# Optimization experiments

Hardware: AMD Instinct MI355X
Metric: run time of the kernel (lower is better)

The kernel has to match this reference:

```python
import jax, jax.numpy as jnp
import numpy as np

HEADS = 4
DIM_HEAD = 32
DIM = 128
EPS = 1e-12  # F.normalize eps


def _rmsnorm(t, g):
    # F.normalize over channel dim (dim=1), then * g * sqrt(dim)
    n = jnp.sqrt(jnp.sum(t * t, axis=1, keepdims=True))
    return t / jnp.maximum(n, EPS) * g * (DIM ** 0.5)


def setup_inputs() -> dict:
    key = jax.random.key(0)
    ks = jax.random.split(key, 5)
    b, H, W = 16, 96, 96
    x = jax.random.normal(ks[0], (b, DIM, H, W), dtype=jnp.float32)
    norm_g = jnp.ones((1, DIM, 1, 1), dtype=jnp.float32)
    qkv_w = jax.random.normal(ks[1], (3 * HEADS * DIM_HEAD, DIM), dtype=jnp.float32) * 0.05
    mem_kv = jax.random.normal(ks[2], (2, HEADS, DIM_HEAD, 4), dtype=jnp.float32)
    out_w = jax.random.normal(ks[3], (DIM, HEADS * DIM_HEAD), dtype=jnp.float32) * 0.05
    out_b = jnp.zeros((DIM,), dtype=jnp.float32)
    out_norm_g = jnp.ones((1, DIM, 1, 1), dtype=jnp.float32)
    return {"x": x, "norm_g": norm_g, "qkv_w": qkv_w, "mem_kv": mem_kv,
            "out_w": out_w, "out_b": out_b, "out_norm_g": out_norm_g}


def reference(x, norm_g, qkv_w, mem_kv, out_w, out_b, out_norm_g):
    b, c, H, W = x.shape
    n = H * W
    scale = DIM_HEAD ** (-0.5)

    xn = _rmsnorm(x, norm_g)
    # 1x1 conv (no bias) == channel GEMM
    qkv = jnp.einsum('oc,bchw->bohw', qkv_w, xn)  # [b, 3*h*d, H, W]
    q, k, v = jnp.split(qkv, 3, axis=1)

    def to_heads(t):
        return t.reshape(b, HEADS, DIM_HEAD, n)  # b h d n

    q, k, v = to_heads(q), to_heads(k), to_heads(v)

    mk = jnp.broadcast_to(mem_kv[0], (b, HEADS, DIM_HEAD, mem_kv.shape[-1]))
    mv = jnp.broadcast_to(mem_kv[1], (b, HEADS, DIM_HEAD, mem_kv.shape[-1]))
    k = jnp.concatenate([mk, k], axis=-1)
    v = jnp.concatenate([mv, v], axis=-1)

    q = jax.nn.softmax(q, axis=-2) * scale  # softmax over d
    k = jax.nn.softmax(k, axis=-1)          # softmax over n

    context = jnp.einsum('bhdn,bhen->bhde', k, v)  # [b,h,d,d]
    out = jnp.einsum('bhde,bhdn->bhen', context, q)  # [b,h,d,n]
    out = out.reshape(b, HEADS * DIM_HEAD, H, W)

    out = jnp.einsum('oc,bchw->bohw', out_w, out) + out_b[None, :, None, None]
    return _rmsnorm(out, out_norm_g)
```

## Files before the change

kernel.cpp:

```cpp
#include <hip/hip_runtime.h>
#include <math.h>

#define NPIX 9216
#define NBLK 72
#define TPB 4
#define SCALE 0.17677669529663687f
#define SQRT128 11.313708498984761f

typedef __attribute__((ext_vector_type(8))) short short8;
typedef __attribute__((ext_vector_type(4))) float f32x4;

static __device__ __forceinline__ unsigned short f2bf(float f) {
  union { float f; unsigned u; } v; v.f = f;
  return (unsigned short)((v.u + 0x7fffu + ((v.u >> 16) & 1u)) >> 16);
}
static __device__ __forceinline__ float bf2f(unsigned short h) {
  union { unsigned u; float f; } v; v.u = ((unsigned)h) << 16;
  return v.f;
}


__global__ __launch_bounds__(256) void k_prep2(
    const float* __restrict__ qkv_w, const float* __restrict__ norm_g,
    const float* __restrict__ out_w,
    unsigned short* __restrict__ wbf2, unsigned short* __restrict__ owb2) {
  const int i = blockIdx.x * 256 + threadIdx.x;
  if (i < 6144) {
    const int g = i >> 6, lane = i & 63;
    const int wv = g / 24, rem = g % 24;
    const int mt = rem >> 2, ks = rem & 3;
    const int row = 96 * wv + mt * 16 + (lane & 15);
    const int col = ks * 32 + (lane >> 4) * 8;
    const float* src = qkv_w + row * 128 + col;
    const float* gg = norm_g + col;
    uint4 o;
    o.x = (unsigned)f2bf(src[0] * gg[0]) | ((unsigned)f2bf(src[1] * gg[1]) << 16);
    o.y = (unsigned)f2bf(src[2] * gg[2]) | ((unsigned)f2bf(src[3] * gg[3]) << 16);
    o.z = (unsigned)f2bf(src[4] * gg[4]) | ((unsigned)f2bf(src[5] * gg[5]) << 16);
    o.w = (unsigned)f2bf(src[6] * gg[6]) | ((unsigned)f2bf(src[7] * gg[7]) << 16);
    *(uint4*)(wbf2 + (size_t)i * 8) = o;
  } else if (i < 8192) {
    const int i2 = i - 6144;
    const int g = i2 >> 6, lane = i2 & 63;
    const int wv = g >> 3, rem = g & 7;
    const int mt = rem >> 2, ks = rem & 3;
    const int row = 32 * wv + mt * 16 + (lane & 15);
    const int col = ks * 32 + (lane >> 4) * 8;
    const float* src = out_w + row * 128 + col;
    uint4 o;
    o.x = (unsigned)f2bf(src[0]) | ((unsigned)f2bf(src[1]) << 16);
    o.y = (unsigned)f2bf(src[2]) | ((unsigned)f2bf(src[3]) << 16);
    o.z = (unsigned)f2bf(src[4]) | ((unsigned)f2bf(src[5]) << 16);
    o.w = (unsigned)f2bf(src[6]) | ((unsigned)f2bf(src[7]) << 16);
    *(uint4*)(owb2 + (size_t)i2 * 8) = o;
  }
}

__global__ __launch_bounds__(256) void k_init(const float* __restrict__ mem_kv,
                                              float* __restrict__ ctxG,
                                              float* __restrict__ sumexpG) {
  const int bh = blockIdx.x;
  const int h = bh & 3;
  const float* mk = mem_kv + h * 128;
  const float* mv = mem_kv + 512 + h * 128;
  const int t = threadIdx.x;
  const int d = t >> 3, e0 = (t & 7) * 4;
  float ek[4], se = 0.f;
#pragma unroll
  for (int j = 0; j < 4; ++j) { ek[j] = __expf(mk[d * 4 + j]); se += ek[j]; }
#pragma unroll
  for (int ei = 0; ei < 4; ++ei) {
    const int e = e0 + ei;
    float s = 0.f;
#pragma unroll
    for (int j = 0; j < 4; ++j) s += ek[j] * mv[e * 4 + j];
    ctxG[(bh * 32 + d) * 32 + e] = s;
  }
  if ((t & 7) == 0) sumexpG[bh * 32 + d] = se;
}

template <bool WSQ>
__global__ __launch_bounds__(256, 2) void k1(
    const float* __restrict__ x, const unsigned short* __restrict__ wbf2,
    unsigned short* __restrict__ qb16, float* __restrict__ qf32,
    float* __restrict__ ctx_dst, float* __restrict__ se_dst) {
  __shared__ __align__(16) unsigned char smem[30720 + 4096 + 128];
  unsigned short* qkv = (unsigned short*)smem;
  unsigned short* xnT = (unsigned short*)smem;
  float* redu = (float*)(smem + 30720);
  float* inv = (float*)(smem + 30720 + 4096);

  const int t = threadIdx.x;
  const int b = blockIdx.y;
  const int blk = blockIdx.x;
  const int wv = t >> 6;
  const int lane = t & 63;
  const int lr = lane & 15;
  const int lg = lane >> 4;
  const int r = t >> 3, c4 = (t & 7) * 4;
  const float* xb = x + ((size_t)b * 128) * NPIX + blk * TPB * 32;

  f32x4 acc[6][2];
  f32x4 ctx[2][2];
#pragma unroll
  for (int i = 0; i < 6; ++i)
#pragma unroll
    for (int j = 0; j < 2; ++j)
#pragma unroll
      for (int q = 0; q < 4; ++q) acc[i][j][q] = 0.f;
#pragma unroll
  for (int i = 0; i < 2; ++i)
#pragma unroll
    for (int j = 0; j < 2; ++j)
#pragma unroll
      for (int q = 0; q < 4; ++q) ctx[i][j][q] = 0.f;
  float se_row[2] = {0.f, 0.f};

  float4 pf[4];
#pragma unroll
  for (int pass = 0; pass < 4; ++pass)
    pf[pass] = *(const float4*)(xb + (size_t)(pass * 32 + r) * NPIX + c4);

  for (int it = 0; it < TPB; ++it) {
    const int p0 = (blk * TPB + it) * 32;

    __syncthreads();
    {
      float ss0 = 0.f, ss1 = 0.f, ss2 = 0.f, ss3 = 0.f;
#pragma unroll
      for (int pass = 0; pass < 4; ++pass) {
        const int row = pass * 32 + r;
        const float4 v = pf[pass];
        xnT[(c4 + 0) * 136 + row] = f2bf(v.x);
        xnT[(c4 + 1) * 136 + row] = f2bf(v.y);
        xnT[(c4 + 2) * 136 + row] = f2bf(v.z);
        xnT[(c4 + 3) * 136 + row] = f2bf(v.w);
        ss0 = fmaf(v.x, v.x, ss0); ss1 = fmaf(v.y, v.y, ss1);
        ss2 = fmaf(v.z, v.z, ss2); ss3 = fmaf(v.w, v.w, ss3);
      }
      *(float4*)&redu[r * 32 + c4] = make_float4(ss0, ss1, ss2, ss3);
    }
    __syncthreads();
    {
      short8 bfr[4][2];
#pragma unroll
      for (int ks = 0; ks < 4; ++ks)
#pragma unroll
        for (int nt = 0; nt < 2; ++nt)
          bfr[ks][nt] = *(const short8*)&xnT[(nt * 16 + lr) * 136 + ks * 32 + lg * 8];
      if (it + 1 < TPB) {
        const float* xb2 = xb + (it + 1) * 32;
#pragma unroll
        for (int pass = 0; pass < 4; ++pass)
          pf[pass] = *(const float4*)(xb2 + (size_t)(pass * 32 + r) * NPIX + c4);
      }
      if (t < 32) {
        float s = 0.f;
#pragma unroll
        for (int g = 0; g < 32; ++g) s += redu[g * 32 + t];
        inv[t] = SQRT128 / fmaxf(sqrtf(s), 1e-12f);
      }
      const unsigned short* wbase = wbf2 + (size_t)(wv * 24) * 512 + lane * 8;
#pragma unroll
      for (int mt = 0; mt < 6; ++mt) {
#pragma unroll
        for (int ks = 0; ks < 4; ++ks) {
          const short8 af = *(const short8*)(wbase + (size_t)(mt * 4 + ks) * 512);
          acc[mt][0] = __builtin_amdgcn_mfma_f32_16x16x32_bf16(af, bfr[ks][0], acc[mt][0], 0, 0, 0);
          acc[mt][1] = __builtin_amdgcn_mfma_f32_16x16x32_bf16(af, bfr[ks][1], acc[mt][1], 0, 0, 0);
        }
      }
    }
    __syncthreads();
    {
      const float iv0 = inv[lr], iv1 = inv[16 + lr];
#pragma unroll
      for (int mt = 0; mt < 6; ++mt)
#pragma unroll
        for (int nt = 0; nt < 2; ++nt) {
          const float iv = nt ? iv1 : iv0;
#pragma unroll
          for (int q = 0; q < 4; ++q) {
            const int row = 96 * wv + mt * 16 + lg * 4 + q;
            qkv[row * 40 + nt * 16 + lr] = f2bf(acc[mt][nt][q] * iv);
            acc[mt][nt][q] = 0.f;
          }
        }
    }
    __syncthreads();
    {
      const int c0 = wv * 32 + lg * 8;
#pragma unroll
      for (int px = 0; px < 2; ++px) {
        const int p = px * 16 + lr;
        float qv[8];
#pragma unroll
        for (int j = 0; j < 8; ++j) qv[j] = bf2f(qkv[(c0 + j) * 40 + p]);
        float m = qv[0];
#pragma unroll
        for (int j = 1; j < 8; ++j) m = fmaxf(m, qv[j]);
        m = fmaxf(m, __shfl_xor(m, 16));
        m = fmaxf(m, __shfl_xor(m, 32));
        float s = 0.f;
#pragma unroll
        for (int j = 0; j < 8; ++j) { qv[j] = __expf(qv[j] - m); s += qv[j]; }
        s += __shfl_xor(s, 16);
        s += __shfl_xor(s, 32);
        const float rs = SCALE / s;
        if (WSQ) {
          uint4 qo;
          qo.x = (unsigned)f2bf(qv[0] * rs) | ((unsigned)f2bf(qv[1] * rs) << 16);
          qo.y = (unsigned)f2bf(qv[2] * rs) | ((unsigned)f2bf(qv[3] * rs) << 16);
          qo.z = (unsigned)f2bf(qv[4] * rs) | ((unsigned)f2bf(qv[5] * rs) << 16);
          qo.w = (unsigned)f2bf(qv[6] * rs) | ((unsigned)f2bf(qv[7] * rs) << 16);
          *(uint4*)(qb16 + ((size_t)b * NPIX + p0 + p) * 128 + c0) = qo;
        } else {
#pragma unroll
          for (int j = 0; j < 8; ++j)
            qf32[((size_t)b * 128 + c0 + j) * NPIX + p0 + p] = qv[j] * rs;
        }
      }
      short8 afk[2];
#pragma unroll
      for (int dt = 0; dt < 2; ++dt) {
        const short8 kraw = *(const short8*)&qkv[(128 + wv * 32 + dt * 16 + lr) * 40 + lg * 8];
        short8 e16;
        float s = 0.f;
#pragma unroll
        for (int j = 0; j < 8; ++j) {
          const float ev = __expf(bf2f((unsigned short)kraw[j]));
          e16[j] = (short)f2bf(ev);
          s += ev;
        }
        afk[dt] = e16;
        s += __shfl_xor(s, 16);
        s += __shfl_xor(s, 32);
        se_row[dt] += s;
      }
#pragma unroll
      for (int dt = 0; dt < 2; ++dt)
#pragma unroll
        for (int et = 0; et < 2; ++et) {
          const short8 bf = *(const short8*)&qkv[(256 + wv * 32 + et * 16 + lr) * 40 + lg * 8];
          ctx[dt][et] = __builtin_amdgcn_mfma_f32_16x16x32_bf16(afk[dt], bf, ctx[dt][et], 0, 0, 0);
        }
    }
  }

  if (WSQ) {
    float* dst = ctx_dst + ((size_t)(b * NBLK + blk)) * 4096 + wv * 1024;
#pragma unroll
    for (int dt = 0; dt < 2; ++dt)
#pragma unroll
      for (int et = 0; et < 2; ++et)
#pragma unroll
        for (int q = 0; q < 4; ++q)
          dst[(dt * 16 + lg * 4 + q) * 32 + et * 16 + lr] = ctx[dt][et][q];
    if (lg == 0) {
#pragma unroll
      for (int dt = 0; dt < 2; ++dt)
        se_dst[(b * NBLK + blk) * 128 + wv * 32 + dt * 16 + lr] = se_row[dt];
    }
  } else {
#pragma unroll
    for (int dt = 0; dt < 2; ++dt)
#pragma unroll
      for (int et = 0; et < 2; ++et)
#pragma unroll
        for (int q = 0; q < 4; ++q)
          atomicAdd(&ctx_dst[((size_t)b * 128 + wv * 32 + dt * 16 + lg * 4 + q) * 32 + et * 16 + lr],
                    ctx[dt][et][q]);
    if (lg == 0) {
#pragma unroll
      for (int dt = 0; dt < 2; ++dt)
        atomicAdd(&se_dst[b * 128 + wv * 32 + dt * 16 + lr], se_row[dt]);
    }
  }
}

__global__ __launch_bounds__(256) void k_reduce(
    const float* __restrict__ part_ctx, const float* __restrict__ part_se,
    const float* __restrict__ mem_kv, unsigned short* __restrict__ ctxnT) {
  const int bid = blockIdx.x;
  const int b = bid >> 4, h = (bid >> 2) & 3, dq = bid & 3;
  const int t = threadIdx.x;
  const int dd = t >> 5;
  const int d = dq * 8 + dd;
  const int e = t & 31;
  __shared__ float sise[8];

  const float* mk = mem_kv + h * 128 + d * 4;
  const float* mv = mem_kv + 512 + h * 128 + e * 4;
  float ek[4];
  float acc = 0.f;
#pragma unroll
  for (int j = 0; j < 4; ++j) ek[j] = __expf(mk[j]);
#pragma unroll
  for (int j = 0; j < 4; ++j) acc += ek[j] * mv[j];
  const float* src = part_ctx + (size_t)b * NBLK * 4096 + h * 1024 + d * 32 + e;
  for (int p = 0; p < NBLK; ++p) acc += src[(size_t)p * 4096];
  if (e == 0) {
    float se = ek[0] + ek[1] + ek[2] + ek[3];
    const float* sp = part_se + (size_t)b * NBLK * 128 + h * 32 + d;
    for (int p = 0; p < NBLK; ++p) se += sp[(size_t)p * 128];
    sise[dd] = 1.f / se;
  }
  __syncthreads();
  ctxnT[(size_t)(b * 4 + h) * 1024 + e * 32 + d] = f2bf(acc * sise[dd]);
}

__global__ __launch_bounds__(256) void k_norm(
    const float* __restrict__ ctxG, const float* __restrict__ seG,
    unsigned short* __restrict__ ctxnT) {
  const int b = blockIdx.x;
  const int t = threadIdx.x;
  const int h = t >> 6, d = (t >> 1) & 31, e0 = (t & 1) * 16;
  const int r = h * 32 + d;
  const float ise = 1.f / seG[b * 128 + r];
  const float* src = ctxG + ((size_t)b * 128 + r) * 32;
  unsigned short* dst = ctxnT + ((size_t)(b * 4 + h) * 32) * 32;
#pragma unroll
  for (int i = 0; i < 16; ++i)
    dst[(e0 + i) * 32 + d] = f2bf(src[e0 + i] * ise);
}

__global__ __launch_bounds__(256) void k3_ws(
    const unsigned short* __restrict__ ctxnT, const unsigned short* __restrict__ owb2,
    const unsigned short* __restrict__ qbf, const float* __restrict__ out_b,
    const float* __restrict__ out_norm_g, float* __restrict__ out) {
  __shared__ __align__(16) unsigned char smem[8704 + 2048 + 128];
  unsigned short* o1T = (unsigned short*)smem;
  float* redu = (float*)(smem + 8704);
  float* inv = (float*)(smem + 8704 + 2048);

  const int t = threadIdx.x;
  const int b = blockIdx.y;
  const int p0 = blockIdx.x * 32;
  const int wv = t >> 6;
  const int lane = t & 63;
  const int lr = lane & 15;
  const int lg = lane >> 4;

  {
    f32x4 o1a[2][2];
#pragma unroll
    for (int i = 0; i < 2; ++i)
#pragma unroll
      for (int j = 0; j < 2; ++j)
#pragma unroll
        for (int q = 0; q < 4; ++q) o1a[i][j][q] = 0.f;
    const unsigned short* cbase = ctxnT + (size_t)(b * 4 + wv) * 1024;
    const unsigned short* qb = qbf + ((size_t)b * NPIX + p0) * 128;
    short8 bq[2];
#pragma unroll
    for (int nt = 0; nt < 2; ++nt)
      bq[nt] = *(const short8*)(qb + (size_t)(nt * 16 + lr) * 128 + wv * 32 + lg * 8);
#pragma unroll
    for (int mt = 0; mt < 2; ++mt) {
      const short8 af = *(const short8*)(cbase + (mt * 16 + lr) * 32 + lg * 8);
#pragma unroll
      for (int nt = 0; nt < 2; ++nt)
        o1a[mt][nt] = __builtin_amdgcn_mfma_f32_16x16x32_bf16(af, bq[nt], o1a[mt][nt], 0, 0, 0);
    }
#pragma unroll
    for (int mt = 0; mt < 2; ++mt)
#pragma unroll
      for (int nt = 0; nt < 2; ++nt)
#pragma unroll
        for (int q = 0; q < 4; ++q) {
          const int e = wv * 32 + mt * 16 + lg * 4 + q;
          o1T[(nt * 16 + lr) * 136 + e] = f2bf(o1a[mt][nt][q]);
        }
  }
  __syncthreads();
  f32x4 y[2][2];
#pragma unroll
  for (int i = 0; i < 2; ++i)
#pragma unroll
    for (int j = 0; j < 2; ++j)
#pragma unroll
      for (int q = 0; q < 4; ++q) y[i][j][q] = 0.f;
  const unsigned short* wbase = owb2 + (size_t)(wv * 8) * 512 + lane * 8;
#pragma unroll
  for (int mt = 0; mt < 2; ++mt) {
#pragma unroll
    for (int ks = 0; ks < 4; ++ks) {
      const short8 af = *(const short8*)(wbase + (size_t)(mt * 4 + ks) * 512);
#pragma unroll
      for (int nt = 0; nt < 2; ++nt) {
        const short8 bf = *(const short8*)&o1T[(nt * 16 + lr) * 136 + ks * 32 + lg * 8];
        y[mt][nt] = __builtin_amdgcn_mfma_f32_16x16x32_bf16(af, bf, y[mt][nt], 0, 0, 0);
      }
    }
  }
  {
    float ss[2] = {0.f, 0.f};
#pragma unroll
    for (int mt = 0; mt < 2; ++mt)
#pragma unroll
      for (int q = 0; q < 4; ++q) {
        const int row = 32 * wv + mt * 16 + lg * 4 + q;
        const float bb = out_b[row];
#pragma unroll
        for (int nt = 0; nt < 2; ++nt) {
          y[mt][nt][q] += bb;
          ss[nt] = fmaf(y[mt][nt][q], y[mt][nt][q], ss[nt]);
        }
      }
#pragma unroll
    for (int nt = 0; nt < 2; ++nt)
      redu[(wv * 4 + lg) * 32 + nt * 16 + lr] = ss[nt];
  }
  __syncthreads();
  if (t < 32) {
    float s = 0.f;
#pragma unroll
    for (int g = 0; g < 16; ++g) s += redu[g * 32 + t];
    inv[t] = SQRT128 / fmaxf(sqrtf(s), 1e-12f);
  }
  __syncthreads();
  {
    float* ob = out + (size_t)b * 128 * NPIX + p0;
#pragma unroll
    for (int mt = 0; mt < 2; ++mt)
#pragma unroll
      for (int q = 0; q < 4; ++q) {
        const int row = 32 * wv + mt * 16 + lg * 4 + q;
        const float g = out_norm_g[row];
#pragma unroll
        for (int nt = 0; nt < 2; ++nt) {
          const int col = nt * 16 + lr;
          ob[(size_t)row * NPIX + col] = y[mt][nt][q] * inv[col] * g;
        }
      }
  }
}

__global__ __launch_bounds__(256) void k3f(
    const unsigned short* __restrict__ ctxnT, const unsigned short* __restrict__ owb2,
    const float* __restrict__ out_b, const float* __restrict__ out_norm_g,
    float* __restrict__ io) {
  __shared__ __align__(16) unsigned char smem[8704 + 8704 + 2048 + 128];
  unsigned short* qT = (unsigned short*)smem;
  unsigned short* o1T = (unsigned short*)(smem + 8704);
  float* redu = (float*)(smem + 8704 + 8704);
  float* inv = (float*)(smem + 8704 + 8704 + 2048);

  const int t = threadIdx.x;
  const int b = blockIdx.y;
  const int p0 = blockIdx.x * 32;
  const int wv = t >> 6;
  const int lane = t & 63;
  const int lr = lane & 15;
  const int lg = lane >> 4;

  {
    const float* qb = io + (size_t)b * 128 * NPIX + p0;
    const int r = t >> 3, c4 = (t & 7) * 4;
#pragma unroll
    for (int pass = 0; pass < 4; ++pass) {
      const int row = pass * 32 + r;
      const float4 v = *(const float4*)(qb + (size_t)row * NPIX + c4);
      qT[(c4 + 0) * 136 + row] = f2bf(v.x);
      qT[(c4 + 1) * 136 + row] = f2bf(v.y);
      qT[(c4 + 2) * 136 + row] = f2bf(v.z);
      qT[(c4 + 3) * 136 + row] = f2bf(v.w);
    }
  }
  __syncthreads();
  {
    f32x4 o1a[2][2];
#pragma unroll
    for (int i = 0; i < 2; ++i)
#pragma unroll
      for (int j = 0; j < 2; ++j)
#pragma unroll
        for (int q = 0; q < 4; ++q) o1a[i][j][q] = 0.f;
    const unsigned short* cbase = ctxnT + (size_t)(b * 4 + wv) * 1024;
#pragma unroll
    for (int mt = 0; mt < 2; ++mt) {
      const short8 af = *(const short8*)(cbase + (mt * 16 + lr) * 32 + lg * 8);
#pragma unroll
      for (int nt = 0; nt < 2; ++nt) {
        const short8 bf = *(const short8*)&qT[(nt * 16 + lr) * 136 + wv * 32 + lg * 8];
        o1a[mt][nt] = __builtin_amdgcn_mfma_f32_16x16x32_bf16(af, bf, o1a[mt][nt], 0, 0, 0);
      }
    }
#pragma unroll
    for (int mt = 0; mt < 2; ++mt)
#pragma unroll
      for (int nt = 0; nt < 2; ++nt)
#pragma unroll
        for (int q = 0; q < 4; ++q) {
          const int e = wv * 32 + mt * 16 + lg * 4 + q;
          o1T[(nt * 16 + lr) * 136 + e] = f2bf(o1a[mt][nt][q]);
        }
  }
  __syncthreads();
  f32x4 y[2][2];
#pragma unroll
  for (int i = 0; i < 2; ++i)
#pragma unroll
    for (int j = 0; j < 2; ++j)
#pragma unroll
      for (int q = 0; q < 4; ++q) y[i][j][q] = 0.f;
  const unsigned short* wbase = owb2 + (size_t)(wv * 8) * 512 + lane * 8;
#pragma unroll
  for (int mt = 0; mt < 2; ++mt) {
#pragma unroll
    for (int ks = 0; ks < 4; ++ks) {
      const short8 af = *(const short8*)(wbase + (size_t)(mt * 4 + ks) * 512);
#pragma unroll
      for (int nt = 0; nt < 2; ++nt) {
        const short8 bf = *(const short8*)&o1T[(nt * 16 + lr) * 136 + ks * 32 + lg * 8];
        y[mt][nt] = __builtin_amdgcn_mfma_f32_16x16x32_bf16(af, bf, y[mt][nt], 0, 0, 0);
      }
    }
  }
  {
    float ss[2] = {0.f, 0.f};
#pragma unroll
    for (int mt = 0; mt < 2; ++mt)
#pragma unroll
      for (int q = 0; q < 4; ++q) {
        const int row = 32 * wv + mt * 16 + lg * 4 + q;
        const float bb = out_b[row];
#pragma unroll
        for (int nt = 0; nt < 2; ++nt) {
          y[mt][nt][q] += bb;
          ss[nt] = fmaf(y[mt][nt][q], y[mt][nt][q], ss[nt]);
        }
      }
#pragma unroll
    for (int nt = 0; nt < 2; ++nt)
      redu[(wv * 4 + lg) * 32 + nt * 16 + lr] = ss[nt];
  }
  __syncthreads();
  if (t < 32) {
    float s = 0.f;
#pragma unroll
    for (int g = 0; g < 16; ++g) s += redu[g * 32 + t];
    inv[t] = SQRT128 / fmaxf(sqrtf(s), 1e-12f);
  }
  __syncthreads();
  {
    float* ob = io + (size_t)b * 128 * NPIX + p0;
#pragma unroll
    for (int mt = 0; mt < 2; ++mt)
#pragma unroll
      for (int q = 0; q < 4; ++q) {
        const int row = 32 * wv + mt * 16 + lg * 4 + q;
        const float g = out_norm_g[row];
#pragma unroll
        for (int nt = 0; nt < 2; ++nt) {
          const int col = nt * 16 + lr;
          ob[(size_t)row * NPIX + col] = y[mt][nt][q] * inv[col] * g;
        }
      }
  }
}

extern "C" void kernel_launch(void* const* d_in, const int* in_sizes, int n_in,
                              void* d_out, int out_size, void* d_ws, size_t ws_size,
                              hipStream_t stream) {
  const float* x          = (const float*)d_in[0];
  const float* norm_g     = (const float*)d_in[1];
  const float* qkv_w      = (const float*)d_in[2];
  const float* mem_kv     = (const float*)d_in[3];
  const float* out_w      = (const float*)d_in[4];
  const float* out_b      = (const float*)d_in[5];
  const float* out_norm_g = (const float*)d_in[6];
  float* out = (float*)d_out;

  const size_t PC = (size_t)16 * NBLK * 4096;
  const size_t PS = (size_t)16 * NBLK * 128;
  const size_t QB = (size_t)16 * NPIX * 128;
  const size_t need = (PC + PS) * 4 + (49152 + 16384 + 65536 + QB) * 2;

  if (ws_size >= need) {
    float* part_ctx = (float*)d_ws;
    float* part_se  = part_ctx + PC;
    unsigned short* wbf2  = (unsigned short*)(part_se + PS);
    unsigned short* owb2  = wbf2 + 49152;
    unsigned short* ctxnT = owb2 + 16384;
    unsigned short* qbf   = ctxnT + 65536;
    k_prep2<<<32, 256, 0, stream>>>(qkv_w, norm_g, out_w, wbf2, owb2);
    k1<true><<<dim3(NBLK, 16), 256, 0, stream>>>(x, wbf2, qbf, nullptr, part_ctx, part_se);
    k_reduce<<<256, 256, 0, stream>>>(part_ctx, part_se, mem_kv, ctxnT);
    k3_ws<<<dim3(288, 16), 256, 0, stream>>>(ctxnT, owb2, qbf, out_b, out_norm_g, out);
  } else {
    float* ctxG = (float*)d_ws;
    float* seG  = ctxG + 65536;
    unsigned short* wbf2  = (unsigned short*)(seG + 2048);
    unsigned short* owb2  = wbf2 + 49152;
    unsigned short* ctxnT = owb2 + 16384;
    k_prep2<<<32, 256, 0, stream>>>(qkv_w, norm_g, out_w, wbf2, owb2);
    k_init<<<64, 256, 0, stream>>>(mem_kv, ctxG, seG);
    k1<false><<<dim3(NBLK, 16), 256, 0, stream>>>(x, wbf2, nullptr, out, ctxG, seG);
    k_norm<<<16, 256, 0, stream>>>(ctxG, seG, ctxnT);
    k3f<<<dim3(288, 16), 256, 0, stream>>>(ctxnT, owb2, out_b, out_norm_g, out);
  }
}
```

Baseline: 83.81 us.

## Separate xnT smem buffer, relayout q to MFMA fragment order, retune tile count

The q intermediate is now stored in per-tile, per-wave MFMA fragment order, so k3 reads its B operands with fully contiguous lane loads instead of strided rows. The x staging buffer in k1 is moved out of the aliased qkv region, which lets the loop-top barrier be dropped. Work per block goes from 4 tiles to 6, with 48 blocks per batch. The bf16 conversions now use the HIP intrinsics. Shared memory per block grows, and removing the barrier relies on the separate buffer being enough to avoid cross-iteration races (the elided section may hold other hazards). There are also fewer blocks, which may reduce occupancy and parallelism.

Result: faster. 77.42 us (-7.6%).

```diff
diff --git a/kernel.cpp b/kernel.cpp
--- a/kernel.cpp
+++ b/kernel.cpp
@@ -1,9 +1,11 @@
 #include <hip/hip_runtime.h>
+#include <hip/hip_bf16.h>
 #include <math.h>
 
 #define NPIX 9216
-#define NBLK 72
-#define TPB 4
+#define NBLK 48
+#define TPB 6
+#define NTILE 288
 #define SCALE 0.17677669529663687f
 #define SQRT128 11.313708498984761f
 
@@ -11,12 +13,10 @@
 typedef __attribute__((ext_vector_type(4))) float f32x4;
 
 static __device__ __forceinline__ unsigned short f2bf(float f) {
-  union { float f; unsigned u; } v; v.f = f;
-  return (unsigned short)((v.u + 0x7fffu + ((v.u >> 16) & 1u)) >> 16);
+  return __bfloat16_as_ushort(__float2bfloat16(f));
 }
 static __device__ __forceinline__ float bf2f(unsigned short h) {
-  union { unsigned u; float f; } v; v.u = ((unsigned)h) << 16;
-  return v.f;
+  return __bfloat162float(__ushort_as_bfloat16(h));
 }
 
 
@@ -84,11 +84,11 @@
     const float* __restrict__ x, const unsigned short* __restrict__ wbf2,
     unsigned short* __restrict__ qb16, float* __restrict__ qf32,
     float* __restrict__ ctx_dst, float* __restrict__ se_dst) {
-  __shared__ __align__(16) unsigned char smem[30720 + 4096 + 128];
+  __shared__ __align__(16) unsigned char smem[30720 + 8704 + 4096 + 128];
   unsigned short* qkv = (unsigned short*)smem;
-  unsigned short* xnT = (unsigned short*)smem;
-  float* redu = (float*)(smem + 30720);
-  float* inv = (float*)(smem + 30720 + 4096);
+  unsigned short* xnT = (unsigned short*)(smem + 30720);
+  float* redu = (float*)(smem + 30720 + 8704);
+  float* inv = (float*)(smem + 30720 + 8704 + 4096);
 
   const int t = threadIdx.x;
   const int b = blockIdx.y;
@@ -122,9 +122,8 @@
     pf[pass] = *(const float4*)(xb + (size_t)(pass * 32 + r) * NPIX + c4);
 
   for (int it = 0; it < TPB; ++it) {
-    const int p0 = (blk * TPB + it) * 32;
-
-    __syncthreads();
+    const int tile = blk * TPB + it;
+
     {
       float ss0 = 0.f, ss1 = 0.f, ss2 = 0.f, ss3 = 0.f;
 #pragma unroll
@@ -213,11 +212,12 @@
           qo.y = (unsigned)f2bf(qv[2] * rs) | ((unsigned)f2bf(qv[3] * rs) << 16);
           qo.z = (unsigned)f2bf(qv[4] * rs) | ((unsigned)f2bf(qv[5] * rs) << 16);
           qo.w = (unsigned)f2bf(qv[6] * rs) | ((unsigned)f2bf(qv[7] * rs) << 16);
-          *(uint4*)(qb16 + ((size_t)b * NPIX + p0 + p) * 128 + c0) = qo;
+          *(uint4*)(qb16 +
+              ((((size_t)(b * NTILE + tile) * 4 + wv) * 2 + px) * 64 + lane) * 8) = qo;
         } else {
 #pragma unroll
           for (int j = 0; j < 8; ++j)
-            qf32[((size_t)b * 128 + c0 + j) * NPIX + p0 + p] = qv[j] * rs;
+            qf32[((size_t)b * 128 + c0 + j) * NPIX + tile * 32 + p] = qv[j] * rs;
         }
       }
       short8 afk[2];
@@ -335,7 +335,8 @@
 
   const int t = threadIdx.x;
   const int b = blockIdx.y;
-  const int p0 = blockIdx.x * 32;
+  const int tile = blockIdx.x;
+  const int p0 = tile * 32;
   const int wv = t >> 6;
   const int lane = t & 63;
   const int lr = lane & 15;
@@ -350,11 +351,11 @@
 #pragma unroll
         for (int q = 0; q < 4; ++q) o1a[i][j][q] = 0.f;
     const unsigned short* cbase = ctxnT + (size_t)(b * 4 + wv) * 1024;
-    const unsigned short* qb = qbf + ((size_t)b * NPIX + p0) * 128;
+    const unsigned short* qb = qbf + (((size_t)(b * NTILE + tile) * 4 + wv) * 2) * 512;
     short8 bq[2];
 #pragma unroll
     for (int nt = 0; nt < 2; ++nt)
-      bq[nt] = *(const short8*)(qb + (size_t)(nt * 16 + lr) * 128 + wv * 32 + lg * 8);
+      bq[nt] = *(const short8*)(qb + (size_t)(nt * 64 + lane) * 8);
 #pragma unroll
     for (int mt = 0; mt < 2; ++mt) {
       const short8 af = *(const short8*)(cbase + (mt * 16 + lr) * 32 + lg * 8);
@@ -587,7 +588,7 @@
     k_prep2<<<32, 256, 0, stream>>>(qkv_w, norm_g, out_w, wbf2, owb2);
     k1<true><<<dim3(NBLK, 16), 256, 0, stream>>>(x, wbf2, qbf, nullptr, part_ctx, part_se);
     k_reduce<<<256, 256, 0, stream>>>(part_ctx, part_se, mem_kv, ctxnT);
-    k3_ws<<<dim3(288, 16), 256, 0, stream>>>(ctxnT, owb2, qbf, out_b, out_norm_g, out);
+    k3_ws<<<dim3(NTILE, 16), 256, 0, stream>>>(ctxnT, owb2, qbf, out_b, out_norm_g, out);
   } else {
     float* ctxG = (float*)d_ws;
     float* seG  = ctxG + 65536;
@@ -598,6 +599,6 @@
     k_init<<<64, 256, 0, stream>>>(mem_kv, ctxG, seG);
     k1<false><<<dim3(NBLK, 16), 256, 0, stream>>>(x, wbf2, nullptr, out, ctxG, seG);
     k_norm<<<16, 256, 0, stream>>>(ctxG, seG, ctxnT);
-    k3f<<<dim3(288, 16), 256, 0, stream>>>(ctxnT, owb2, out_b, out_norm_g, out);
-  }
-}
+    k3f<<<dim3(NTILE, 16), 256, 0, stream>>>(ctxnT, owb2, out_b, out_norm_g, out);
+  }
+}
```
